# Kernel optimization log

Measured on AMD Instinct MI355X. Metric: run time of the kernel, lower is better.

The kernel has to match this reference:

```python
import jax, jax.numpy as jnp
import numpy as np
from jax import lax

N_KERNELS = 11
N_GRAMS = 3
EMB = 300
CONV_OUT = 128
B, QLEN, DLEN = 128, 30, 256


def _kernel_mus(n):
    mus = [1.0]
    bin_size = 2.0 / (n - 1)
    mus.append(1 - bin_size / 2)
    for i in range(1, n - 1):
        mus.append(mus[i] - bin_size)
    return mus


def _kernel_sigmas(n):
    bin_size = 2.0 / (n - 1)
    return [0.001] + [0.5 * bin_size] * (n - 1)


MU = jnp.asarray(np.array(_kernel_mus(N_KERNELS), dtype=np.float32))      # [K]
SIGMA = jnp.asarray(np.array(_kernel_sigmas(N_KERNELS), dtype=np.float32))  # [K]


def setup_inputs() -> dict:
    key = jax.random.key(0)
    ks = jax.random.split(key, 10)
    inp = {
        "query_embeddings": jax.random.normal(ks[0], (B, QLEN, EMB), jnp.float32),
        "document_embeddings": jax.random.normal(ks[1], (B, DLEN, EMB), jnp.float32),
        "query_pad_oov_mask": jnp.ones((B, QLEN), jnp.float32),
        "document_pad_oov_mask": jnp.ones((B, DLEN), jnp.float32),
    }
    # conv weights for n-gram sizes 1..3: [out_ch, in_ch, ksize]
    for i in range(1, N_GRAMS + 1):
        inp[f"conv_w{i}"] = jax.random.normal(ks[1 + i], (CONV_OUT, EMB, i), jnp.float32) * 0.05
        inp[f"conv_b{i}"] = jnp.zeros((CONV_OUT,), jnp.float32)
    inp["dense_w"] = jax.random.uniform(ks[9], (1, N_KERNELS * N_GRAMS * N_GRAMS), jnp.float32,
                                        minval=-0.014, maxval=0.014)
    return inp


def _conv_ngram(x, w, b):
    # x: [B, L, E]; w: [C, E, k]; right-pad by k-1 so output length == L (ConstantPad1d((0,k-1)))
    k = w.shape[-1]
    y = lax.conv_general_dilated(x.transpose(0, 2, 1), w, (1,), [(0, k - 1)],
                                 dimension_numbers=("NCH", "OIH", "NCH"))
    return jax.nn.relu(y + b[None, :, None]).transpose(0, 2, 1)  # [B, L, C]


def _kernel_pool(q, d, qd_mask, q_mask):
    # cosine matrix (AllenNLP CosineMatrixAttention: normalize with +1e-13 eps)
    qn = q / (jnp.linalg.norm(q, axis=-1, keepdims=True) + 1e-13)
    dn = d / (jnp.linalg.norm(d, axis=-1, keepdims=True) + 1e-13)
    cos = jnp.einsum("bqe,bde->bqd", qn, dn) * qd_mask  # [B, Q, D]
    # RBF soft-histogram kernels: [B, Q, D, K]
    k = jnp.exp(-(cos[..., None] - MU) ** 2 / (2.0 * SIGMA ** 2)) * qd_mask[..., None]
    per_kernel_query = k.sum(axis=2)  # [B, Q, K]
    log_pk = jnp.log(jnp.clip(per_kernel_query, 1e-10, None)) * 0.01
    return (log_pk * q_mask[..., None]).sum(axis=1)  # [B, K]


def reference(query_embeddings, document_embeddings, query_pad_oov_mask, document_pad_oov_mask,
              conv_w1, conv_b1, conv_w2, conv_b2, conv_w3, conv_b3, dense_w):
    qd_mask = query_pad_oov_mask[:, :, None] * document_pad_oov_mask[:, None, :]  # [B, Q, D]
    conv_params = [(conv_w1, conv_b1), (conv_w2, conv_b2), (conv_w3, conv_b3)]
    q_res = [_conv_ngram(query_embeddings, w, b) for w, b in conv_params]
    d_res = [_conv_ngram(document_embeddings, w, b) for w, b in conv_params]
    matched = [_kernel_pool(q_res[i], d_res[t], qd_mask, query_pad_oov_mask)
               for i in range(N_GRAMS) for t in range(N_GRAMS)]
    all_grams = jnp.concatenate(matched, axis=1)  # [B, K*9]
    return jnp.squeeze(all_grams @ dense_w.T, axis=1)  # [B]
```

## Files before the change

kernel.cpp:

```cpp
#include <hip/hip_runtime.h>
#include <math.h>


typedef __bf16 bf16x8 __attribute__((ext_vector_type(8)));
typedef float f32x4 __attribute__((ext_vector_type(4)));

#if __has_builtin(__builtin_amdgcn_exp2f)
#define EXP2F(x) __builtin_amdgcn_exp2f(x)
#else
#define EXP2F(x) exp2f(x)
#endif

#define AS_STRIDE 344

static __device__ __forceinline__ unsigned short f2bf(float f) {
  union { float f; unsigned int u; } v; v.f = f;
  unsigned int r = v.u + 0x7FFFu + ((v.u >> 16) & 1u);
  return (unsigned short)(r >> 16);
}

__global__ __launch_bounds__(256) void prep_w(
    const float* __restrict__ w1, const float* __restrict__ w2,
    const float* __restrict__ w3, unsigned short* __restrict__ wt2) {
  int idx = blockIdx.x * 256 + threadIdx.x;
  if (idx >= 245760) return;
  int jj   = idx & 7;
  int lane = (idx >> 3) & 63;
  int ec   = (idx >> 9) % 10;
  int cb   = (idx / 5120) & 7;
  int p    = idx / 40960;
  const float* w; int k, jt;
  if (p == 0)      { w = w1; k = 1; jt = 0; }
  else if (p <= 2) { w = w2; k = 2; jt = p - 1; }
  else             { w = w3; k = 3; jt = p - 3; }
  int c = cb * 16 + (lane & 15);
  int e = ec * 32 + (lane >> 4) * 8 + jj;
  float v = (e < 300) ? w[(c * 300 + e) * k + jt] : 0.0f;
  wt2[idx] = f2bf(v);
}

__global__ __launch_bounds__(256) void prep_x(
    const float* __restrict__ qemb, const float* __restrict__ demb,
    unsigned short* __restrict__ qx, unsigned short* __restrict__ dx) {
  int idx = blockIdx.x * 256 + threadIdx.x;
  if (idx >= 1474560) return;
  int c8   = idx % 40;
  int ridx = idx / 40;
  const float* src; unsigned short* dst; int valid;
  if (ridx < 4096) {
    int b = ridx >> 5, r = ridx & 31;
    valid = (r < 30);
    src = qemb + ((size_t)b * 30 + r) * 300;
    dst = qx + (size_t)ridx * 320;
  } else {
    int rd = ridx - 4096;
    valid = 1;
    src = demb + (size_t)rd * 300;
    dst = dx + (size_t)rd * 320;
  }
  int e = c8 * 8;
  float4 a = make_float4(0.f, 0.f, 0.f, 0.f);
  float4 c = make_float4(0.f, 0.f, 0.f, 0.f);
  if (valid && e < 300)     a = *reinterpret_cast<const float4*>(src + e);
  if (valid && e + 4 < 300) c = *reinterpret_cast<const float4*>(src + e + 4);
  uint4 o;
  o.x = (unsigned int)f2bf(a.x) | ((unsigned int)f2bf(a.y) << 16);
  o.y = (unsigned int)f2bf(a.z) | ((unsigned int)f2bf(a.w) << 16);
  o.z = (unsigned int)f2bf(c.x) | ((unsigned int)f2bf(c.y) << 16);
  o.w = (unsigned int)f2bf(c.z) | ((unsigned int)f2bf(c.w) << 16);
  *reinterpret_cast<uint4*>(dst + e) = o;
}

__global__ __launch_bounds__(256) void conv_all(
    const unsigned short* __restrict__ qx, const unsigned short* __restrict__ dx,
    const unsigned short* __restrict__ wt2,
    const float* __restrict__ b1, const float* __restrict__ b2,
    const float* __restrict__ b3,
    unsigned short* __restrict__ qn, unsigned short* __restrict__ dn) {
  __shared__ unsigned short As[34 * AS_STRIDE];
  __shared__ float psq[4][3][32];

  const int bi = blockIdx.x;
  const unsigned short* xs; unsigned short* out;
  int L, Lpad, b, l0;
  if (bi >= 1024) {
    b = bi - 1024; l0 = 0; L = 30; Lpad = 32;
    xs = qx + (size_t)b * 32 * 320; out = qn;
  } else {
    b = bi >> 3; l0 = (bi & 7) * 32; L = 256; Lpad = 256;
    xs = dx + (size_t)b * 256 * 320; out = dn;
  }

  const int t = threadIdx.x;
  const int w = __builtin_amdgcn_readfirstlane(t >> 6);
  const int lane = t & 63;
  const int quad = lane >> 4, lrow = lane & 15;

  for (int idx = t; idx < 34 * 40; idx += 256) {
    int r = idx / 40, c = idx % 40;
    int l = l0 + r;
    uint4 v = make_uint4(0u, 0u, 0u, 0u);
    if (l < Lpad) v = *reinterpret_cast<const uint4*>(xs + (size_t)l * 320 + c * 8);
    *reinterpret_cast<uint4*>(&As[r * AS_STRIDE + c * 8]) = v;
  }
  __syncthreads();

  f32x4 acc[2][6];
  #pragma unroll
  for (int ni = 0; ni < 2; ++ni)
    #pragma unroll
    for (int nt = 0; nt < 6; ++nt) acc[ni][nt] = (f32x4){0.f, 0.f, 0.f, 0.f};

  const unsigned short* wl = wt2 + lane * 8;

  #pragma unroll 2
  for (int ec = 0; ec < 10; ++ec) {
    #pragma unroll
    for (int j = 0; j < 3; ++j) {
      bf16x8 xf[2];
      #pragma unroll
      for (int ni = 0; ni < 2; ++ni)
        xf[ni] = *reinterpret_cast<const bf16x8*>(
            &As[(ni * 16 + lrow + j) * AS_STRIDE + ec * 32 + quad * 8]);
      #pragma unroll
      for (int nt = 0; nt < 6; ++nt) {
        const int g = nt >> 1;
        if (j <= g) {
          const int cb = (nt & 1) * 4 + w;
          const int pst = (g * (g + 1)) >> 1;
          bf16x8 wf = *reinterpret_cast<const bf16x8*>(
              wl + ((((pst + j) * 8 + cb) * 10 + ec) << 9));
          acc[0][nt] = __builtin_amdgcn_mfma_f32_16x16x32_bf16(
              wf, xf[0], acc[0][nt], 0, 0, 0);
          acc[1][nt] = __builtin_amdgcn_mfma_f32_16x16x32_bf16(
              wf, xf[1], acc[1][nt], 0, 0, 0);
        }
      }
    }
  }

  const float* biases[3] = {b1, b2, b3};
  float4 bv[6];
  #pragma unroll
  for (int nt = 0; nt < 6; ++nt)
    bv[nt] = *reinterpret_cast<const float4*>(
        biases[nt >> 1] + ((nt & 1) * 4 + w) * 16 + quad * 4);

  #pragma unroll
  for (int ni = 0; ni < 2; ++ni) {
    float p[3] = {0.f, 0.f, 0.f};
    #pragma unroll
    for (int nt = 0; nt < 6; ++nt) {
      #pragma unroll
      for (int r = 0; r < 4; ++r) {
        float y = fmaxf(acc[ni][nt][r] + bv[nt][r], 0.f);
        p[nt >> 1] += y * y;
      }
    }
    #pragma unroll
    for (int g = 0; g < 3; ++g) {
      float v = p[g];
      v += __shfl_xor(v, 16);
      v += __shfl_xor(v, 32);
      if (lane < 16) psq[w][g][ni * 16 + lrow] = v;
    }
  }
  __syncthreads();

  #pragma unroll
  for (int ni = 0; ni < 2; ++ni) {
    int row = ni * 16 + lrow;
    int l = l0 + row;
    if (l < L) {
      float inv[3];
      #pragma unroll
      for (int g = 0; g < 3; ++g)
        inv[g] = 1.0f / (sqrtf(psq[0][g][row] + psq[1][g][row] +
                               psq[2][g][row] + psq[3][g][row]) + 1e-13f);
      #pragma unroll
      for (int nt = 0; nt < 6; ++nt) {
        const int g = nt >> 1;
        unsigned int pk[2];
        #pragma unroll
        for (int h = 0; h < 2; ++h) {
          float y0 = fmaxf(acc[ni][nt][2 * h + 0] + bv[nt][2 * h + 0], 0.f) * inv[g];
          float y1 = fmaxf(acc[ni][nt][2 * h + 1] + bv[nt][2 * h + 1], 0.f) * inv[g];
          pk[h] = (unsigned int)f2bf(y0) | ((unsigned int)f2bf(y1) << 16);
        }
        unsigned short* op = out + ((size_t)(g * 128 + b) * L + l) * 128 +
                             ((nt & 1) * 4 + w) * 16 + quad * 4;
        *reinterpret_cast<uint2*>(op) = make_uint2(pk[0], pk[1]);
      }
    }
  }
}

__global__ __launch_bounds__(64) void pool_mfma(
    const unsigned short* __restrict__ qn, const unsigned short* __restrict__ dn,
    const float* __restrict__ qmask, const float* __restrict__ dmask,
    float* __restrict__ pkq8) {
  const float MU[11] = {1.0f, 0.9f, 0.7f, 0.5f, 0.3f, 0.1f,
                        -0.1f, -0.3f, -0.5f, -0.7f, -0.9f};
  const float NEGC[11] = {-721347.52f, -72.134752f, -72.134752f, -72.134752f,
                          -72.134752f, -72.134752f, -72.134752f, -72.134752f,
                          -72.134752f, -72.134752f, -72.134752f};
  const int tg    = blockIdx.x >> 3;
  const int chunk = blockIdx.x & 7;
  const int b     = blockIdx.y;
  const int lane  = threadIdx.x;
  const int quad  = lane >> 4, l15 = lane & 15;
  const int d0    = chunk * 32;

  const unsigned short* dslab = dn + (size_t)(tg * 128 + b) * 256 * 128;

  bf16x8 aD[2][4];
  #pragma unroll
  for (int mi = 0; mi < 2; ++mi)
    #pragma unroll
    for (int kt = 0; kt < 4; ++kt)
      aD[mi][kt] = *reinterpret_cast<const bf16x8*>(
          dslab + (size_t)(d0 + mi * 16 + l15) * 128 + kt * 32 + quad * 8);

  float dmv[2][4];
  #pragma unroll
  for (int mi = 0; mi < 2; ++mi)
    #pragma unroll
    for (int r = 0; r < 4; ++r)
      dmv[mi][r] = dmask[b * 256 + d0 + mi * 16 + quad * 4 + r];

  float qmv[2];
  qmv[0] = qmask[b * 30 + l15];
  qmv[1] = (16 + l15 < 30) ? qmask[b * 30 + 16 + l15] : 0.0f;

  #pragma unroll 1
  for (int ig = 0; ig < 3; ++ig) {
    const unsigned short* qslab = qn + (size_t)(ig * 128 + b) * 30 * 128;

    bf16x8 bQ[2][4];
    #pragma unroll
    for (int ni = 0; ni < 2; ++ni)
      #pragma unroll
      for (int kt = 0; kt < 4; ++kt)
        bQ[ni][kt] = *reinterpret_cast<const bf16x8*>(
            qslab + (size_t)(ni * 16 + l15) * 128 + kt * 32 + quad * 8);

    f32x4 acc[2][2];
    #pragma unroll
    for (int mi = 0; mi < 2; ++mi)
      #pragma unroll
      for (int ni = 0; ni < 2; ++ni) acc[mi][ni] = (f32x4){0.f, 0.f, 0.f, 0.f};

    #pragma unroll
    for (int kt = 0; kt < 4; ++kt)
      #pragma unroll
      for (int mi = 0; mi < 2; ++mi)
        #pragma unroll
        for (int ni = 0; ni < 2; ++ni)
          acc[mi][ni] = __builtin_amdgcn_mfma_f32_16x16x32_bf16(
              aD[mi][kt], bQ[ni][kt], acc[mi][ni], 0, 0, 0);

    float feat[2][11];
    #pragma unroll
    for (int ni = 0; ni < 2; ++ni)
      #pragma unroll
      for (int kk = 0; kk < 11; ++kk) feat[ni][kk] = 0.0f;

    #pragma unroll
    for (int mi = 0; mi < 2; ++mi) {
      #pragma unroll
      for (int r = 0; r < 4; ++r) {
        #pragma unroll
        for (int ni = 0; ni < 2; ++ni) {
          float m  = qmv[ni] * dmv[mi][r];
          float cm = acc[mi][ni][r] * m;
          #pragma unroll
          for (int kk = 0; kk < 11; ++kk) {
            float d2 = cm - MU[kk];
            feat[ni][kk] += EXP2F(d2 * d2 * NEGC[kk]) * m;
          }
        }
      }
    }

    #pragma unroll
    for (int ni = 0; ni < 2; ++ni)
      #pragma unroll
      for (int kk = 0; kk < 11; ++kk) {
        float v = feat[ni][kk];
        v += __shfl_xor(v, 16);
        v += __shfl_xor(v, 32);
        feat[ni][kk] = v;
      }

    if (quad == 0) {
      const int pair = ig * 3 + tg;
      #pragma unroll
      for (int ni = 0; ni < 2; ++ni) {
        int q = ni * 16 + l15;
        if (q < 30) {
          float* p = pkq8 +
              (((size_t)(chunk * 9 + pair) * 128 + b) * 30 + q) * 11;
          #pragma unroll
          for (int kk = 0; kk < 11; ++kk) p[kk] = feat[ni][kk];
        }
      }
    }
  }
}

__global__ __launch_bounds__(256) void final_kernel(
    const float* __restrict__ pkq8, const float* __restrict__ qmask,
    const float* __restrict__ dw, float* __restrict__ out) {
  const int CH = 9 * 128 * 30 * 11;
  const int b = blockIdx.x;
  const int t = threadIdx.x;
  float s = 0.0f;
  for (int idx = t; idx < 9 * 30 * 11; idx += 256) {
    int pair = idx / 330;
    int rem  = idx % 330;
    int q    = rem / 11;
    int kk   = rem % 11;
    size_t base = (((size_t)pair * 128 + b) * 30 + q) * 11 + kk;
    float v = 0.f;
    #pragma unroll
    for (int c = 0; c < 8; ++c) v += pkq8[base + (size_t)c * CH];
    s += __logf(fmaxf(v, 1e-10f)) * 0.01f * qmask[b * 30 + q] * dw[pair * 11 + kk];
  }
  s += __shfl_xor(s, 1);  s += __shfl_xor(s, 2);  s += __shfl_xor(s, 4);
  s += __shfl_xor(s, 8);  s += __shfl_xor(s, 16); s += __shfl_xor(s, 32);
  __shared__ float part[4];
  if ((t & 63) == 0) part[t >> 6] = s;
  __syncthreads();
  if (t == 0) out[b] = part[0] + part[1] + part[2] + part[3];
}

extern "C" void kernel_launch(void* const* d_in, const int* in_sizes, int n_in,
                              void* d_out, int out_size, void* d_ws, size_t ws_size,
                              hipStream_t stream) {
  const float* qemb  = (const float*)d_in[0];
  const float* demb  = (const float*)d_in[1];
  const float* qmask = (const float*)d_in[2];
  const float* dmask = (const float*)d_in[3];
  const float* w1 = (const float*)d_in[4];
  const float* b1 = (const float*)d_in[5];
  const float* w2 = (const float*)d_in[6];
  const float* b2 = (const float*)d_in[7];
  const float* w3 = (const float*)d_in[8];
  const float* b3 = (const float*)d_in[9];
  const float* dw = (const float*)d_in[10];

  unsigned short* ws   = (unsigned short*)d_ws;
  unsigned short* wt2  = ws;
  unsigned short* qx   = ws + 245760;
  unsigned short* dx   = ws + 1556480;
  unsigned short* qn   = ws + 12042240;
  unsigned short* dn   = ws + 13516800;
  float*          pkq8 = (float*)(ws + 245760);

  prep_w<<<960, 256, 0, stream>>>(w1, w2, w3, wt2);
  prep_x<<<5760, 256, 0, stream>>>(qemb, demb, qx, dx);
  conv_all<<<1152, 256, 0, stream>>>(qx, dx, wt2, b1, b2, b3, qn, dn);
  pool_mfma<<<dim3(24, 128), 64, 0, stream>>>(qn, dn, qmask, dmask, pkq8);
  final_kernel<<<128, 256, 0, stream>>>(pkq8, qmask, dw, (float*)d_out);
}
```

Measured before the change: 181.2 us.

## Merge prep kernels, enlarge conv tiles, fuse pooling with final reduction

Folds the weight and embedding bf16 conversion into one prep launch, which also zeroes the output. The conv kernel moves to 512-thread blocks: each wave owns 16 channels for all three n-gram sizes, and doc blocks cover 64 rows, so more MFMA work reuses each staged LDS tile. Pooling and the final log/dense reduction are fused: per-query histograms accumulate in shared memory via atomics across 8 waves, and each block atomically adds its partial dot product into the output. This removes two launches and the pkq8 global round-trip, at the cost of LDS atomics, non-deterministic float summation order, and fewer, larger pool blocks (384 instead of 3072).

```diff
diff --git a/kernel.cpp b/kernel.cpp
--- a/kernel.cpp
+++ b/kernel.cpp
@@ -19,197 +19,204 @@
   return (unsigned short)(r >> 16);
 }
 
-__global__ __launch_bounds__(256) void prep_w(
+__global__ __launch_bounds__(256) void prep(
     const float* __restrict__ w1, const float* __restrict__ w2,
-    const float* __restrict__ w3, unsigned short* __restrict__ wt2) {
-  int idx = blockIdx.x * 256 + threadIdx.x;
-  if (idx >= 245760) return;
-  int jj   = idx & 7;
-  int lane = (idx >> 3) & 63;
-  int ec   = (idx >> 9) % 10;
-  int cb   = (idx / 5120) & 7;
-  int p    = idx / 40960;
-  const float* w; int k, jt;
-  if (p == 0)      { w = w1; k = 1; jt = 0; }
-  else if (p <= 2) { w = w2; k = 2; jt = p - 1; }
-  else             { w = w3; k = 3; jt = p - 3; }
-  int c = cb * 16 + (lane & 15);
-  int e = ec * 32 + (lane >> 4) * 8 + jj;
-  float v = (e < 300) ? w[(c * 300 + e) * k + jt] : 0.0f;
-  wt2[idx] = f2bf(v);
-}
-
-__global__ __launch_bounds__(256) void prep_x(
+    const float* __restrict__ w3,
     const float* __restrict__ qemb, const float* __restrict__ demb,
-    unsigned short* __restrict__ qx, unsigned short* __restrict__ dx) {
-  int idx = blockIdx.x * 256 + threadIdx.x;
-  if (idx >= 1474560) return;
-  int c8   = idx % 40;
-  int ridx = idx / 40;
-  const float* src; unsigned short* dst; int valid;
-  if (ridx < 4096) {
-    int b = ridx >> 5, r = ridx & 31;
-    valid = (r < 30);
-    src = qemb + ((size_t)b * 30 + r) * 300;
-    dst = qx + (size_t)ridx * 320;
+    unsigned short* __restrict__ wt2,
+    unsigned short* __restrict__ qx, unsigned short* __restrict__ dx,
+    float* __restrict__ out) {
+  const int bid = blockIdx.x;
+  const int t = threadIdx.x;
+  if (bid < 960) {
+    int idx = bid * 256 + t;
+    if (idx >= 245760) return;
+    int jj   = idx & 7;
+    int lane = (idx >> 3) & 63;
+    int ec   = (idx >> 9) % 10;
+    int cb   = (idx / 5120) & 7;
+    int p    = idx / 40960;
+    const float* w; int k, jt;
+    if (p == 0)      { w = w1; k = 1; jt = 0; }
+    else if (p <= 2) { w = w2; k = 2; jt = p - 1; }
+    else             { w = w3; k = 3; jt = p - 3; }
+    int c = cb * 16 + (lane & 15);
+    int e = ec * 32 + (lane >> 4) * 8 + jj;
+    float v = (e < 300) ? w[(c * 300 + e) * k + jt] : 0.0f;
+    wt2[idx] = f2bf(v);
+  } else if (bid < 6720) {
+    int idx = (bid - 960) * 256 + t;
+    if (idx >= 1474560) return;
+    int c8   = idx % 40;
+    int ridx = idx / 40;
+    const float* src; unsigned short* dst; int valid;
+    if (ridx < 4096) {
+      int b = ridx >> 5, r = ridx & 31;
+      valid = (r < 30);
+      src = qemb + ((size_t)b * 30 + r) * 300;
+      dst = qx + (size_t)ridx * 320;
+    } else {
+      int rd = ridx - 4096;
+      valid = 1;
+      src = demb + (size_t)rd * 300;
+      dst = dx + (size_t)rd * 320;
+    }
+    int e = c8 * 8;
+    float4 a = make_float4(0.f, 0.f, 0.f, 0.f);
+    float4 c = make_float4(0.f, 0.f, 0.f, 0.f);
+    if (valid && e < 300)     a = *reinterpret_cast<const float4*>(src + e);
+    if (valid && e + 4 < 300) c = *reinterpret_cast<const float4*>(src + e + 4);
+    uint4 o;
+    o.x = (unsigned int)f2bf(a.x) | ((unsigned int)f2bf(a.y) << 16);
+    o.y = (unsigned int)f2bf(a.z) | ((unsigned int)f2bf(a.w) << 16);
+    o.z = (unsigned int)f2bf(c.x) | ((unsigned int)f2bf(c.y) << 16);
+    o.w = (unsigned int)f2bf(c.z) | ((unsigned int)f2bf(c.w) << 16);
+    *reinterpret_cast<uint4*>(dst + e) = o;
   } else {
-    int rd = ridx - 4096;
-    valid = 1;
-    src = demb + (size_t)rd * 300;
-    dst = dx + (size_t)rd * 320;
-  }
-  int e = c8 * 8;
-  float4 a = make_float4(0.f, 0.f, 0.f, 0.f);
-  float4 c = make_float4(0.f, 0.f, 0.f, 0.f);
-  if (valid && e < 300)     a = *reinterpret_cast<const float4*>(src + e);
-  if (valid && e + 4 < 300) c = *reinterpret_cast<const float4*>(src + e + 4);
-  uint4 o;
-  o.x = (unsigned int)f2bf(a.x) | ((unsigned int)f2bf(a.y) << 16);
-  o.y = (unsigned int)f2bf(a.z) | ((unsigned int)f2bf(a.w) << 16);
-  o.z = (unsigned int)f2bf(c.x) | ((unsigned int)f2bf(c.y) << 16);
-  o.w = (unsigned int)f2bf(c.z) | ((unsigned int)f2bf(c.w) << 16);
-  *reinterpret_cast<uint4*>(dst + e) = o;
-}
-
-__global__ __launch_bounds__(256) void conv_all(
+    if (t < 128) out[t] = 0.0f;
+  }
+}
+
+template<int NI>
+__device__ __forceinline__ void conv_body(
+    unsigned short* As, float* psq,
+    const unsigned short* __restrict__ xs, int L, int Lpad, int l0, int b,
+    const unsigned short* __restrict__ wt2,
+    const float* __restrict__ b1, const float* __restrict__ b2,
+    const float* __restrict__ b3,
+    unsigned short* __restrict__ out) {
+  constexpr int ROWS = NI * 16 + 2;
+  constexpr int NR = NI * 16;
+  const int t = threadIdx.x;
+  const int w = __builtin_amdgcn_readfirstlane(t >> 6);
+  const int lane = t & 63;
+  const int quad = lane >> 4, lrow = lane & 15;
+
+  for (int idx = t; idx < ROWS * 40; idx += 512) {
+    int r = idx / 40, c = idx % 40;
+    int l = l0 + r;
+    uint4 v = make_uint4(0u, 0u, 0u, 0u);
+    if (l < Lpad) v = *reinterpret_cast<const uint4*>(xs + (size_t)l * 320 + c * 8);
+    *reinterpret_cast<uint4*>(&As[r * AS_STRIDE + c * 8]) = v;
+  }
+  __syncthreads();
+
+  f32x4 acc[NI][3];
+  #pragma unroll
+  for (int ni = 0; ni < NI; ++ni)
+    #pragma unroll
+    for (int g = 0; g < 3; ++g) acc[ni][g] = (f32x4){0.f, 0.f, 0.f, 0.f};
+
+  const unsigned short* wl = wt2 + (size_t)lane * 8;
+
+  #pragma unroll 2
+  for (int ec = 0; ec < 10; ++ec) {
+    #pragma unroll
+    for (int j = 0; j < 3; ++j) {
+      bf16x8 xf[NI];
+      #pragma unroll
+      for (int ni = 0; ni < NI; ++ni)
+        xf[ni] = *reinterpret_cast<const bf16x8*>(
+            &As[(ni * 16 + lrow + j) * AS_STRIDE + ec * 32 + quad * 8]);
+      #pragma unroll
+      for (int g = j; g < 3; ++g) {
+        const int pst = (g * (g + 1)) >> 1;
+        bf16x8 wf = *reinterpret_cast<const bf16x8*>(
+            wl + ((((pst + j) * 8 + w) * 10 + ec) << 9));
+        #pragma unroll
+        for (int ni = 0; ni < NI; ++ni)
+          acc[ni][g] = __builtin_amdgcn_mfma_f32_16x16x32_bf16(
+              wf, xf[ni], acc[ni][g], 0, 0, 0);
+      }
+    }
+  }
+
+  const float* biases[3] = {b1, b2, b3};
+  float4 bv[3];
+  #pragma unroll
+  for (int g = 0; g < 3; ++g)
+    bv[g] = *reinterpret_cast<const float4*>(biases[g] + w * 16 + quad * 4);
+
+  #pragma unroll
+  for (int ni = 0; ni < NI; ++ni) {
+    #pragma unroll
+    for (int g = 0; g < 3; ++g) {
+      float p = 0.f;
+      #pragma unroll
+      for (int r = 0; r < 4; ++r) {
+        float y = fmaxf(acc[ni][g][r] + bv[g][r], 0.f);
+        p += y * y;
+      }
+      p += __shfl_xor(p, 16);
+      p += __shfl_xor(p, 32);
+      if (lane < 16) psq[(w * 3 + g) * NR + ni * 16 + lrow] = p;
+    }
+  }
+  __syncthreads();
+
+  #pragma unroll
+  for (int ni = 0; ni < NI; ++ni) {
+    int row = ni * 16 + lrow;
+    int l = l0 + row;
+    if (l < L) {
+      #pragma unroll
+      for (int g = 0; g < 3; ++g) {
+        float ssq = 0.f;
+        #pragma unroll
+        for (int wv = 0; wv < 8; ++wv) ssq += psq[(wv * 3 + g) * NR + row];
+        float inv = 1.0f / (sqrtf(ssq) + 1e-13f);
+        unsigned int pk[2];
+        #pragma unroll
+        for (int h = 0; h < 2; ++h) {
+          float y0 = fmaxf(acc[ni][g][2 * h + 0] + bv[g][2 * h + 0], 0.f) * inv;
+          float y1 = fmaxf(acc[ni][g][2 * h + 1] + bv[g][2 * h + 1], 0.f) * inv;
+          pk[h] = (unsigned int)f2bf(y0) | ((unsigned int)f2bf(y1) << 16);
+        }
+        unsigned short* op = out + ((size_t)(g * 128 + b) * L + l) * 128 +
+                             w * 16 + quad * 4;
+        *reinterpret_cast<uint2*>(op) = make_uint2(pk[0], pk[1]);
+      }
+    }
+  }
+}
+
+__global__ __launch_bounds__(512, 4) void conv_all(
     const unsigned short* __restrict__ qx, const unsigned short* __restrict__ dx,
     const unsigned short* __restrict__ wt2,
     const float* __restrict__ b1, const float* __restrict__ b2,
     const float* __restrict__ b3,
     unsigned short* __restrict__ qn, unsigned short* __restrict__ dn) {
-  __shared__ unsigned short As[34 * AS_STRIDE];
-  __shared__ float psq[4][3][32];
-
+  __shared__ unsigned short As[66 * AS_STRIDE];
+  __shared__ float psq[8 * 3 * 64];
   const int bi = blockIdx.x;
-  const unsigned short* xs; unsigned short* out;
-  int L, Lpad, b, l0;
-  if (bi >= 1024) {
-    b = bi - 1024; l0 = 0; L = 30; Lpad = 32;
-    xs = qx + (size_t)b * 32 * 320; out = qn;
-  } else {
-    b = bi >> 3; l0 = (bi & 7) * 32; L = 256; Lpad = 256;
-    xs = dx + (size_t)b * 256 * 320; out = dn;
-  }
-
-  const int t = threadIdx.x;
-  const int w = __builtin_amdgcn_readfirstlane(t >> 6);
-  const int lane = t & 63;
-  const int quad = lane >> 4, lrow = lane & 15;
-
-  for (int idx = t; idx < 34 * 40; idx += 256) {
-    int r = idx / 40, c = idx % 40;
-    int l = l0 + r;
-    uint4 v = make_uint4(0u, 0u, 0u, 0u);
-    if (l < Lpad) v = *reinterpret_cast<const uint4*>(xs + (size_t)l * 320 + c * 8);
-    *reinterpret_cast<uint4*>(&As[r * AS_STRIDE + c * 8]) = v;
-  }
-  __syncthreads();
-
-  f32x4 acc[2][6];
-  #pragma unroll
-  for (int ni = 0; ni < 2; ++ni)
-    #pragma unroll
-    for (int nt = 0; nt < 6; ++nt) acc[ni][nt] = (f32x4){0.f, 0.f, 0.f, 0.f};
-
-  const unsigned short* wl = wt2 + lane * 8;
-
-  #pragma unroll 2
-  for (int ec = 0; ec < 10; ++ec) {
-    #pragma unroll
-    for (int j = 0; j < 3; ++j) {
-      bf16x8 xf[2];
-      #pragma unroll
-      for (int ni = 0; ni < 2; ++ni)
-        xf[ni] = *reinterpret_cast<const bf16x8*>(
-            &As[(ni * 16 + lrow + j) * AS_STRIDE + ec * 32 + quad * 8]);
-      #pragma unroll
-      for (int nt = 0; nt < 6; ++nt) {
-        const int g = nt >> 1;
-        if (j <= g) {
-          const int cb = (nt & 1) * 4 + w;
-          const int pst = (g * (g + 1)) >> 1;
-          bf16x8 wf = *reinterpret_cast<const bf16x8*>(
-              wl + ((((pst + j) * 8 + cb) * 10 + ec) << 9));
-          acc[0][nt] = __builtin_amdgcn_mfma_f32_16x16x32_bf16(
-              wf, xf[0], acc[0][nt], 0, 0, 0);
-          acc[1][nt] = __builtin_amdgcn_mfma_f32_16x16x32_bf16(
-              wf, xf[1], acc[1][nt], 0, 0, 0);
-        }
-      }
-    }
-  }
-
-  const float* biases[3] = {b1, b2, b3};
-  float4 bv[6];
-  #pragma unroll
-  for (int nt = 0; nt < 6; ++nt)
-    bv[nt] = *reinterpret_cast<const float4*>(
-        biases[nt >> 1] + ((nt & 1) * 4 + w) * 16 + quad * 4);
-
-  #pragma unroll
-  for (int ni = 0; ni < 2; ++ni) {
-    float p[3] = {0.f, 0.f, 0.f};
-    #pragma unroll
-    for (int nt = 0; nt < 6; ++nt) {
-      #pragma unroll
-      for (int r = 0; r < 4; ++r) {
-        float y = fmaxf(acc[ni][nt][r] + bv[nt][r], 0.f);
-        p[nt >> 1] += y * y;
-      }
-    }
-    #pragma unroll
-    for (int g = 0; g < 3; ++g) {
-      float v = p[g];
-      v += __shfl_xor(v, 16);
-      v += __shfl_xor(v, 32);
-      if (lane < 16) psq[w][g][ni * 16 + lrow] = v;
-    }
-  }
-  __syncthreads();
-
-  #pragma unroll
-  for (int ni = 0; ni < 2; ++ni) {
-    int row = ni * 16 + lrow;
-    int l = l0 + row;
-    if (l < L) {
-      float inv[3];
-      #pragma unroll
-      for (int g = 0; g < 3; ++g)
-        inv[g] = 1.0f / (sqrtf(psq[0][g][row] + psq[1][g][row] +
-                               psq[2][g][row] + psq[3][g][row]) + 1e-13f);
-      #pragma unroll
-      for (int nt = 0; nt < 6; ++nt) {
-        const int g = nt >> 1;
-        unsigned int pk[2];
-        #pragma unroll
-        for (int h = 0; h < 2; ++h) {
-          float y0 = fmaxf(acc[ni][nt][2 * h + 0] + bv[nt][2 * h + 0], 0.f) * inv[g];
-          float y1 = fmaxf(acc[ni][nt][2 * h + 1] + bv[nt][2 * h + 1], 0.f) * inv[g];
-          pk[h] = (unsigned int)f2bf(y0) | ((unsigned int)f2bf(y1) << 16);
-        }
-        unsigned short* op = out + ((size_t)(g * 128 + b) * L + l) * 128 +
-                             ((nt & 1) * 4 + w) * 16 + quad * 4;
-        *reinterpret_cast<uint2*>(op) = make_uint2(pk[0], pk[1]);
-      }
-    }
-  }
-}
-
-__global__ __launch_bounds__(64) void pool_mfma(
+  if (bi < 512)
+    conv_body<4>(As, psq, dx + (size_t)(bi >> 2) * 256 * 320, 256, 256,
+                 (bi & 3) * 64, bi >> 2, wt2, b1, b2, b3, dn);
+  else
+    conv_body<2>(As, psq, qx + (size_t)(bi - 512) * 32 * 320, 30, 32,
+                 0, bi - 512, wt2, b1, b2, b3, qn);
+}
+
+__global__ __launch_bounds__(512) void pool_final(
     const unsigned short* __restrict__ qn, const unsigned short* __restrict__ dn,
     const float* __restrict__ qmask, const float* __restrict__ dmask,
-    float* __restrict__ pkq8) {
+    const float* __restrict__ dw, float* __restrict__ out) {
   const float MU[11] = {1.0f, 0.9f, 0.7f, 0.5f, 0.3f, 0.1f,
                         -0.1f, -0.3f, -0.5f, -0.7f, -0.9f};
   const float NEGC[11] = {-721347.52f, -72.134752f, -72.134752f, -72.134752f,
                           -72.134752f, -72.134752f, -72.134752f, -72.134752f,
                           -72.134752f, -72.134752f, -72.134752f};
-  const int tg    = blockIdx.x >> 3;
-  const int chunk = blockIdx.x & 7;
-  const int b     = blockIdx.y;
-  const int lane  = threadIdx.x;
-  const int quad  = lane >> 4, l15 = lane & 15;
-  const int d0    = chunk * 32;
+  __shared__ float pf[3 * 30 * 11];
+  __shared__ float part[8];
+
+  const int tg = blockIdx.x;
+  const int b  = blockIdx.y;
+  const int t  = threadIdx.x;
+  const int wv = t >> 6, lane = t & 63;
+  const int quad = lane >> 4, l15 = lane & 15;
+  const int d0 = wv * 32;
+
+  for (int idx = t; idx < 990; idx += 512) pf[idx] = 0.f;
 
   const unsigned short* dslab = dn + (size_t)(tg * 128 + b) * 256 * 128;
 
@@ -231,6 +238,8 @@
   float qmv[2];
   qmv[0] = qmask[b * 30 + l15];
   qmv[1] = (16 + l15 < 30) ? qmask[b * 30 + 16 + l15] : 0.0f;
+
+  __syncthreads();
 
   #pragma unroll 1
   for (int ig = 0; ig < 3; ++ig) {
@@ -293,45 +302,39 @@
       }
 
     if (quad == 0) {
-      const int pair = ig * 3 + tg;
       #pragma unroll
       for (int ni = 0; ni < 2; ++ni) {
         int q = ni * 16 + l15;
         if (q < 30) {
-          float* p = pkq8 +
-              (((size_t)(chunk * 9 + pair) * 128 + b) * 30 + q) * 11;
           #pragma unroll
-          for (int kk = 0; kk < 11; ++kk) p[kk] = feat[ni][kk];
+          for (int kk = 0; kk < 11; ++kk)
+            atomicAdd(&pf[(ig * 30 + q) * 11 + kk], feat[ni][kk]);
         }
       }
     }
   }
-}
-
-__global__ __launch_bounds__(256) void final_kernel(
-    const float* __restrict__ pkq8, const float* __restrict__ qmask,
-    const float* __restrict__ dw, float* __restrict__ out) {
-  const int CH = 9 * 128 * 30 * 11;
-  const int b = blockIdx.x;
-  const int t = threadIdx.x;
-  float s = 0.0f;
-  for (int idx = t; idx < 9 * 30 * 11; idx += 256) {
-    int pair = idx / 330;
-    int rem  = idx % 330;
-    int q    = rem / 11;
-    int kk   = rem % 11;
-    size_t base = (((size_t)pair * 128 + b) * 30 + q) * 11 + kk;
-    float v = 0.f;
-    #pragma unroll
-    for (int c = 0; c < 8; ++c) v += pkq8[base + (size_t)c * CH];
-    s += __logf(fmaxf(v, 1e-10f)) * 0.01f * qmask[b * 30 + q] * dw[pair * 11 + kk];
+  __syncthreads();
+
+  float s = 0.f;
+  for (int idx = t; idx < 990; idx += 512) {
+    int ig = idx / 330;
+    int rem = idx % 330;
+    int q  = rem / 11;
+    int kk = rem % 11;
+    float v = pf[idx];
+    s += __logf(fmaxf(v, 1e-10f)) * 0.01f * qmask[b * 30 + q] *
+         dw[(ig * 3 + tg) * 11 + kk];
   }
   s += __shfl_xor(s, 1);  s += __shfl_xor(s, 2);  s += __shfl_xor(s, 4);
   s += __shfl_xor(s, 8);  s += __shfl_xor(s, 16); s += __shfl_xor(s, 32);
-  __shared__ float part[4];
-  if ((t & 63) == 0) part[t >> 6] = s;
-  __syncthreads();
-  if (t == 0) out[b] = part[0] + part[1] + part[2] + part[3];
+  if (lane == 0) part[wv] = s;
+  __syncthreads();
+  if (t == 0) {
+    float tot = 0.f;
+    #pragma unroll
+    for (int i = 0; i < 8; ++i) tot += part[i];
+    atomicAdd(&out[b], tot);
+  }
 }
 
 extern "C" void kernel_launch(void* const* d_in, const int* in_sizes, int n_in,
@@ -349,17 +352,15 @@
   const float* b3 = (const float*)d_in[9];
   const float* dw = (const float*)d_in[10];
 
-  unsigned short* ws   = (unsigned short*)d_ws;
-  unsigned short* wt2  = ws;
-  unsigned short* qx   = ws + 245760;
-  unsigned short* dx   = ws + 1556480;
-  unsigned short* qn   = ws + 12042240;
-  unsigned short* dn   = ws + 13516800;
-  float*          pkq8 = (float*)(ws + 245760);
-
-  prep_w<<<960, 256, 0, stream>>>(w1, w2, w3, wt2);
-  prep_x<<<5760, 256, 0, stream>>>(qemb, demb, qx, dx);
-  conv_all<<<1152, 256, 0, stream>>>(qx, dx, wt2, b1, b2, b3, qn, dn);
-  pool_mfma<<<dim3(24, 128), 64, 0, stream>>>(qn, dn, qmask, dmask, pkq8);
-  final_kernel<<<128, 256, 0, stream>>>(pkq8, qmask, dw, (float*)d_out);
-}
+  unsigned short* ws  = (unsigned short*)d_ws;
+  unsigned short* wt2 = ws;
+  unsigned short* qx  = ws + 245760;
+  unsigned short* dx  = ws + 1556480;
+  unsigned short* qn  = ws + 12042240;
+  unsigned short* dn  = ws + 13516800;
+  float* out = (float*)d_out;
+
+  prep<<<6721, 256, 0, stream>>>(w1, w2, w3, qemb, demb, wt2, qx, dx, out);
+  conv_all<<<640, 512, 0, stream>>>(qx, dx, wt2, b1, b2, b3, qn, dn);
+  pool_final<<<dim3(3, 128), 512, 0, stream>>>(qn, dn, qmask, dmask, dw, out);
+}
```

Result: no change. 182.7 us (+0.8%).
